# Kernel optimization log

Measured on AMD Instinct MI355X. Metric: run time of the kernel, lower is better.

Reference implementation:

```python
import jax, jax.numpy as jnp
import numpy as np

B, NIN, NREG, D, H, L = 8, 1024, 16, 1024, 16, 12
DFF = 4 * D
S = NIN + NREG
HD = D // H
EPS = 1e-6


def setup_inputs() -> dict:
    key = jax.random.key(0)
    ks = jax.random.split(key, 8)
    p = lambda k, shape: jax.random.normal(k, shape, jnp.float32) * 0.02
    return dict(
        x=jax.random.normal(ks[0], (B, S, D), jnp.float32),
        n_input=NIN,
        ln1_g=jnp.ones((L, D), jnp.float32), ln1_b=jnp.zeros((L, D), jnp.float32),
        wqkv=p(ks[1], (L, D, 3 * D)), bqkv=jnp.zeros((L, 3 * D), jnp.float32),
        wo=p(ks[2], (L, D, D)), bo=jnp.zeros((L, D), jnp.float32),
        ln2_g=jnp.ones((L, D), jnp.float32), ln2_b=jnp.zeros((L, D), jnp.float32),
        w1=p(ks[3], (L, D, DFF)), b1=jnp.zeros((L, DFF), jnp.float32),
        w2=p(ks[4], (L, DFF, D)), b2=jnp.zeros((L, D), jnp.float32),
        lnf_g=jnp.ones((D,), jnp.float32), lnf_b=jnp.zeros((D,), jnp.float32),
    )


def _ln(x, g, b):
    mu = x.mean(-1, keepdims=True)
    var = ((x - mu) ** 2).mean(-1, keepdims=True)
    return (x - mu) * jax.lax.rsqrt(var + EPS) * g + b


def _build_mask(n_input, total):
    # inputs attend everywhere; registers attend to all inputs and causally among registers
    i = jnp.arange(total)[:, None]
    j = jnp.arange(total)[None, :]
    blocked = (i >= n_input) & (j >= n_input) & (j > i)
    return jnp.where(blocked, -jnp.inf, 0.0).astype(jnp.float32)  # (S, S) additive


def _attn(h, wqkv_l, bqkv_l, wo_l, bo_l, mask):
    b, s, _ = h.shape
    qkv = h @ wqkv_l + bqkv_l                                   # (B,S,3D)
    q, k, v = jnp.split(qkv, 3, axis=-1)
    q = q.reshape(b, s, H, HD).transpose(0, 2, 1, 3)            # (B,H,S,HD)
    k = k.reshape(b, s, H, HD).transpose(0, 2, 1, 3)
    v = v.reshape(b, s, H, HD).transpose(0, 2, 1, 3)
    scores = jnp.einsum('bhqd,bhkd->bhqk', q, k) / np.sqrt(HD) + mask
    a = jax.nn.softmax(scores, axis=-1)
    o = jnp.einsum('bhqk,bhkd->bhqd', a, v)
    o = o.transpose(0, 2, 1, 3).reshape(b, s, D)
    return o @ wo_l + bo_l


def reference(x, n_input, ln1_g, ln1_b, wqkv, bqkv, wo, bo,
              ln2_g, ln2_b, w1, b1, w2, b2, lnf_g, lnf_b):
    mask = _build_mask(n_input, x.shape[1])

    def blk(h, p):
        l1g, l1b, wq, bq, wo_, bo_, l2g, l2b, w1_, b1_, w2_, b2_ = p
        h = h + _attn(_ln(h, l1g, l1b), wq, bq, wo_, bo_, mask)
        u = _ln(h, l2g, l2b) @ w1_ + b1_
        h = h + jax.nn.gelu(u) @ w2_ + b2_
        return h, None

    h, _ = jax.lax.scan(blk, x, (ln1_g, ln1_b, wqkv, bqkv, wo, bo,
                                 ln2_g, ln2_b, w1, b1, w2, b2))
    return _ln(h, lnf_g, lnf_b)
```

## Files before the change

### kernel.cpp

```cpp
#include <hip/hip_runtime.h>
#include <hip/hip_bf16.h>
#include <stdint.h>

#define DD   1024
#define TD   3072
#define DFFN 4096
#define NL   12
#define SS   1040
#define SP   1056
#define BB   8
#define MM   (BB*SS)
#define HH   16
#define NTAIL 16

typedef float  f32x4  __attribute__((ext_vector_type(4)));
typedef __bf16 bf16x8 __attribute__((ext_vector_type(8)));
typedef unsigned short u16;

union Bf8 { bf16x8 v; u16 s[8]; };

__device__ __forceinline__ u16 f2b(float f) {
  union { float f; unsigned u; } x; x.f = f;
  unsigned r = (x.u + 0x7FFFu + ((x.u >> 16) & 1u)) >> 16;
  return (u16)r;
}

__device__ __forceinline__ f32x4 mfma_bf16(bf16x8 a, bf16x8 b, f32x4 c) {
  return __builtin_amdgcn_mfma_f32_16x16x32_bf16(a, b, c, 0, 0, 0);
}

__device__ __forceinline__ void gload_lds16(const u16* g, u16* l) {
  __builtin_amdgcn_global_load_lds((const __attribute__((address_space(1))) void*)g,
                                   (__attribute__((address_space(3))) void*)l, 16, 0, 0);
}

__device__ __forceinline__ float dppmax16(float t) {
  union { float f; int i; } u, v;
  u.f = t;
  v.i = __builtin_amdgcn_update_dpp(0, u.i, 0xB1, 0xF, 0xF, true);
  u.f = fmaxf(u.f, v.f);
  v.i = __builtin_amdgcn_update_dpp(0, u.i, 0x4E, 0xF, 0xF, true);
  u.f = fmaxf(u.f, v.f);
  v.i = __builtin_amdgcn_update_dpp(0, u.i, 0x124, 0xF, 0xF, true);
  u.f = fmaxf(u.f, v.f);
  v.i = __builtin_amdgcn_update_dpp(0, u.i, 0x128, 0xF, 0xF, true);
  u.f = fmaxf(u.f, v.f);
  return u.f;
}

__global__ __launch_bounds__(256)
void transpose_cast(const float* __restrict__ in, u16* __restrict__ out, int K, int N) {
  __shared__ float tile[32][33];
  const int n0 = blockIdx.x * 32, k0 = blockIdx.y * 32;
  const size_t lb = (size_t)blockIdx.z * K * N;
  const int tx = threadIdx.x, ty = threadIdx.y;
  for (int j = 0; j < 4; ++j)
    tile[ty + 8*j][tx] = in[lb + (size_t)(k0 + ty + 8*j) * N + n0 + tx];
  __syncthreads();
  for (int j = 0; j < 4; ++j)
    out[lb + (size_t)(n0 + ty + 8*j) * K + k0 + tx] = f2b(tile[tx][ty + 8*j]);
}

template<int OUTF>
__global__ __launch_bounds__(256)
void ln_kernel(const float* __restrict__ in, const float* __restrict__ gam,
               const float* __restrict__ bet, u16* __restrict__ outb, float* __restrict__ outf) {
  const int row = blockIdx.x, t = threadIdx.x;
  const float4 v = ((const float4*)(in + (size_t)row * DD))[t];
  float s  = v.x + v.y + v.z + v.w;
  float s2 = v.x*v.x + v.y*v.y + v.z*v.z + v.w*v.w;
  for (int off = 1; off < 64; off <<= 1) { s += __shfl_xor(s, off); s2 += __shfl_xor(s2, off); }
  __shared__ float red[8];
  if ((t & 63) == 0) { red[t >> 6] = s; red[4 + (t >> 6)] = s2; }
  __syncthreads();
  s  = red[0] + red[1] + red[2] + red[3];
  s2 = red[4] + red[5] + red[6] + red[7];
  const float mu = s * (1.0f/1024.0f);
  const float var = s2 * (1.0f/1024.0f) - mu*mu;
  const float rs = rsqrtf(var + 1e-6f);
  const float4 gv = ((const float4*)gam)[t];
  const float4 bv = ((const float4*)bet)[t];
  const float y0 = (v.x - mu)*rs*gv.x + bv.x;
  const float y1 = (v.y - mu)*rs*gv.y + bv.y;
  const float y2 = (v.z - mu)*rs*gv.z + bv.z;
  const float y3 = (v.w - mu)*rs*gv.w + bv.w;
  if (OUTF) {
    float4 o; o.x=y0; o.y=y1; o.z=y2; o.w=y3;
    ((float4*)(outf + (size_t)row * DD))[t] = o;
  } else {
    ushort4 o; o.x=f2b(y0); o.y=f2b(y1); o.z=f2b(y2); o.w=f2b(y3);
    ((ushort4*)(outb + (size_t)row * DD))[t] = o;
  }
}

template<int EPI>
__global__ __launch_bounds__(256, 2)
void gemm_bt(const u16* __restrict__ A, const u16* __restrict__ Bt,
             const float* __restrict__ bias,
             u16* outB,
             u16* __restrict__ qb, u16* __restrict__ kb, u16* __restrict__ vtb,
             int N, int K) {
  __shared__ u16 As[128*64];
  __shared__ u16 Bs[128*64];
  const int tid = threadIdx.x;

  const int nwg = gridDim.x * gridDim.y;
  int wgid = blockIdx.y * gridDim.x + blockIdx.x;
  wgid = (wgid & 7) * (nwg >> 3) + (wgid >> 3);
  const int nb = wgid % gridDim.y;
  const int mb = wgid / gridDim.y;
  const int m0 = mb * 128, n0 = nb * 128;

  const int lane = tid & 63, w = tid >> 6;
  const int wr = (w >> 1) * 64, wc = (w & 1) * 64;
  const int c = lane & 15, g = lane >> 4;

  f32x4 acc[4][4];
  for (int i = 0; i < 4; ++i) for (int j = 0; j < 4; ++j) acc[i][j] = f32x4{0.f,0.f,0.f,0.f};

  const int srow = tid >> 3, scg = tid & 7;
  const size_t aoff = (size_t)(m0 + srow) * K + scg * 8;
  const size_t boff = (size_t)(n0 + srow) * K + scg * 8;

  for (int kt = 0; kt < K; kt += 64) {
    for (int it = 0; it < 4; ++it) {
      gload_lds16(A  + aoff + (size_t)it * 32 * K + kt, As + (it*256 + tid) * 8);
      gload_lds16(Bt + boff + (size_t)it * 32 * K + kt, Bs + (it*256 + tid) * 8);
    }
    __syncthreads();
    for (int kk = 0; kk < 2; ++kk) {
      bf16x8 af[4], bfr[4];
      for (int i = 0; i < 4; ++i) af[i]  = *(const bf16x8*)(As + (wr + i*16 + c)*64 + kk*32 + g*8);
      for (int j = 0; j < 4; ++j) bfr[j] = *(const bf16x8*)(Bs + (wc + j*16 + c)*64 + kk*32 + g*8);
      for (int i = 0; i < 4; ++i)
        for (int j = 0; j < 4; ++j)
          acc[i][j] = mfma_bf16(af[i], bfr[j], acc[i][j]);
    }
    __syncthreads();
  }

  for (int j = 0; j < 4; ++j) {
    const int col = n0 + wc + j*16 + c;
    const float bcol = bias[col];
    for (int i = 0; i < 4; ++i) {
      const int row0 = m0 + wr + i*16 + 4*g;
      if (EPI == 3) {
        const int part = col >> 10;
        const int hh2  = (col >> 6) & 15;
        const int hd   = col & 63;
        const int bb   = (int)((unsigned)row0 / SS);
        const int s0   = row0 - bb * SS;
        const size_t bh = (size_t)(bb * HH + hh2);
        if (part == 2) {
          ushort4 pk;
          pk.x = f2b(acc[i][j][0] + bcol);
          pk.y = f2b(acc[i][j][1] + bcol);
          pk.z = f2b(acc[i][j][2] + bcol);
          pk.w = f2b(acc[i][j][3] + bcol);
          *(ushort4*)(vtb + (bh*64 + hd)*SP + s0) = pk;
        } else if (part == 0) {
          for (int r = 0; r < 4; ++r)
            qb[(bh*SP + s0 + r)*64 + hd] = f2b((acc[i][j][r] + bcol) * 0.125f);
        } else {
          for (int r = 0; r < 4; ++r)
            kb[(bh*SP + s0 + r)*64 + hd] = f2b(acc[i][j][r] + bcol);
        }
      } else {
        for (int r = 0; r < 4; ++r) {
          const size_t idx = (size_t)(row0 + r) * N + col;
          const float v = acc[i][j][r] + bcol;
          const float z = 1.5957691216f * (v + 0.044715f * v * v * v);
          const float e = __expf(z);
          outB[idx] = f2b(v * e * __builtin_amdgcn_rcpf(e + 1.0f));
        }
      }
    }
  }
}

__global__ __launch_bounds__(256, 4)
void gemm64(const u16* __restrict__ A, const u16* __restrict__ Bt,
            const float* __restrict__ bias, const float* __restrict__ resid,
            float* __restrict__ outF, int N, int K) {
  __shared__ u16 As[64*64];
  __shared__ u16 Bs[128*64];
  const int tid = threadIdx.x;

  const int nwg = gridDim.x * gridDim.y;
  int wgid = blockIdx.y * gridDim.x + blockIdx.x;
  wgid = (wgid & 7) * (nwg >> 3) + (wgid >> 3);
  const int nb = wgid % gridDim.y;
  const int mb = wgid / gridDim.y;
  const int m0 = mb * 64, n0 = nb * 128;

  const int lane = tid & 63, w = tid >> 6;
  const int wr = (w >> 1) * 32, wc = (w & 1) * 64;
  const int c = lane & 15, g = lane >> 4;

  f32x4 acc[2][4];
  for (int i = 0; i < 2; ++i) for (int j = 0; j < 4; ++j) acc[i][j] = f32x4{0.f,0.f,0.f,0.f};

  const int srow = tid >> 3, scg = tid & 7;
  const size_t aoff = (size_t)(m0 + srow) * K + scg * 8;
  const size_t boff = (size_t)(n0 + srow) * K + scg * 8;

  for (int kt = 0; kt < K; kt += 64) {
    for (int it = 0; it < 2; ++it)
      gload_lds16(A  + aoff + (size_t)it * 32 * K + kt, As + (it*256 + tid) * 8);
    for (int it = 0; it < 4; ++it)
      gload_lds16(Bt + boff + (size_t)it * 32 * K + kt, Bs + (it*256 + tid) * 8);
    __syncthreads();
    for (int kk = 0; kk < 2; ++kk) {
      bf16x8 af[2], bfr[4];
      for (int i = 0; i < 2; ++i) af[i]  = *(const bf16x8*)(As + (wr + i*16 + c)*64 + kk*32 + g*8);
      for (int j = 0; j < 4; ++j) bfr[j] = *(const bf16x8*)(Bs + (wc + j*16 + c)*64 + kk*32 + g*8);
      for (int i = 0; i < 2; ++i)
        for (int j = 0; j < 4; ++j)
          acc[i][j] = mfma_bf16(af[i], bfr[j], acc[i][j]);
    }
    __syncthreads();
  }

  for (int j = 0; j < 4; ++j) {
    const int col = n0 + wc + j*16 + c;
    const float bcol = bias[col];
    for (int i = 0; i < 2; ++i) {
      const int row0 = m0 + wr + i*16 + 4*g;
      for (int r = 0; r < 4; ++r) {
        const size_t idx = (size_t)(row0 + r) * N + col;
        outF[idx] = acc[i][j][r] + bcol + resid[idx];
      }
    }
  }
}

__global__ __launch_bounds__(512, 8)
void attn_staged(const u16* __restrict__ Qb, const u16* __restrict__ Kb,
                 const u16* __restrict__ VTb, u16* __restrict__ out,
                 const int* __restrict__ npt) {
  __shared__ u16 KV[2][4096];
  __shared__ u16 PT[8][640];
  const int tid = threadIdx.x;
  const int w = tid >> 6, lane = tid & 63;
  const int c = lane & 15, g = lane >> 4;
  const int nin = npt[0];
  u16* pw = PT[w];

  if (blockIdx.x < NTAIL) {
    const int bh = blockIdx.x * 8 + w;
    const int b = bh >> 4, hh = bh & 15;
    const int q0 = 64 * 16;

    bf16x8 aq0, aq1;
    {
      const u16* qp = Qb + ((size_t)bh * SP + q0 + c) * 64 + g * 8;
      aq0 = *(const bf16x8*)qp;
      aq1 = *(const bf16x8*)(qp + 32);
    }

    float m[4], ls[4];
    f32x4 o[4];
    int qrow[4];
    for (int r = 0; r < 4; ++r) { m[r] = -1e30f; ls[r] = 0.f; qrow[r] = q0 + 4*g + r; }
    for (int nd = 0; nd < 4; ++nd) o[nd] = f32x4{0.f,0.f,0.f,0.f};

    for (int kt = 0; kt < 33; ++kt) {
      const int k0 = kt * 32;

      f32x4 s[2];
      {
        const u16* kp0 = Kb + ((size_t)bh * SP + k0 + c) * 64 + g * 8;
        f32x4 z0 = f32x4{0.f,0.f,0.f,0.f};
        z0 = mfma_bf16(aq0, *(const bf16x8*)kp0, z0);
        z0 = mfma_bf16(aq1, *(const bf16x8*)(kp0 + 32), z0);
        s[0] = z0;
        const u16* kp1 = kp0 + 16 * 64;
        f32x4 z1 = f32x4{0.f,0.f,0.f,0.f};
        z1 = mfma_bf16(aq0, *(const bf16x8*)kp1, z1);
        z1 = mfma_bf16(aq1, *(const bf16x8*)(kp1 + 32), z1);
        s[1] = z1;
      }

      for (int jt = 0; jt < 2; ++jt) {
        const int j = k0 + jt*16 + c;
        for (int r = 0; r < 4; ++r) {
          const int q = qrow[r];
          const bool blocked = (j >= SS) || ((q >= nin) && (j >= nin) && (j > q));
          if (blocked) s[jt][r] = -1e30f;
        }
      }

      for (int r = 0; r < 4; ++r) {
        float t = fmaxf(s[0][r], s[1][r]);
        for (int off = 1; off < 16; off <<= 1) t = fmaxf(t, __shfl_xor(t, off));
        const float mn = fmaxf(m[r], t);
        const float al = __expf(m[r] - mn);
        m[r] = mn;
        const float p0 = __expf(s[0][r] - mn);
        const float p1 = __expf(s[1][r] - mn);
        s[0][r] = p0; s[1][r] = p1;
        float ps = p0 + p1;
        for (int off = 1; off < 16; off <<= 1) ps += __shfl_xor(ps, off);
        ls[r] = ls[r] * al + ps;
        for (int nd = 0; nd < 4; ++nd) o[nd][r] *= al;
      }

      for (int jt = 0; jt < 2; ++jt)
        for (int r = 0; r < 4; ++r)
          pw[(4*g + r)*40 + jt*16 + c] = f2b(s[jt][r]);
      __builtin_amdgcn_sched_barrier(0);
      bf16x8 ap = *(const bf16x8*)(pw + c*40 + 8*g);
      __builtin_amdgcn_sched_barrier(0);

      for (int nd = 0; nd < 4; ++nd) {
        const u16* vp = VTb + ((size_t)bh * 64 + nd*16 + c) * SP + k0 + 8*g;
        o[nd] = mfma_bf16(ap, *(const bf16x8*)vp, o[nd]);
      }
    }

    for (int nd = 0; nd < 4; ++nd)
      for (int r = 0; r < 4; ++r) {
        const float v = o[nd][r] / ls[r];
        out[((size_t)b * SS + qrow[r]) * DD + hh*64 + nd*16 + c] = f2b(v);
      }
    return;
  }

  const int sb = blockIdx.x - NTAIL;
  const int bh = sb & 127;
  const int qt = (sb >> 7) * 8 + w;
  const int b = bh >> 4, hh = bh & 15;
  const int q0 = qt * 16;

  const u16* ssrc; int kstr; u16* sdst;
  if (tid < 256) {
    const int row = tid >> 3, col8 = (tid & 7) ^ (row & 7);
    ssrc = Kb + ((size_t)bh * SP + row) * 64 + col8 * 8;
    kstr = 32 * 64;
    sdst = &KV[0][tid * 8];
  } else {
    const int t2 = tid - 256, row = t2 >> 2, col8 = (t2 & 3) ^ (row & 3);
    ssrc = VTb + ((size_t)bh * 64 + row) * SP + col8 * 8;
    kstr = 32;
    sdst = &KV[0][2048 + t2 * 8];
  }
#define STAGE(bufbit, kt) gload_lds16(ssrc + (size_t)(kt) * kstr, sdst + (bufbit) * 4096)

  bf16x8 aq0, aq1;
  {
    const u16* qp = Qb + ((size_t)bh * SP + q0 + c) * 64 + g * 8;
    aq0 = *(const bf16x8*)qp;
    aq1 = *(const bf16x8*)(qp + 32);
  }

  Bf8 onesf;
  for (int i = 0; i < 8; ++i) onesf.s[i] = (c == 0) ? (u16)0x3F80 : (u16)0;

  float m[4];
  f32x4 o[5];
  int qrow[4];
  for (int r = 0; r < 4; ++r) { m[r] = -1e30f; qrow[r] = q0 + 4*g + r; }
  for (int nd = 0; nd < 5; ++nd) o[nd] = f32x4{0.f,0.f,0.f,0.f};

  const bool tile_regs = (q0 + 15) >= nin;
  const int c7 = c & 7, c3 = c & 3;

  STAGE(0, 0);

  for (int kt = 0; kt < 33; ++kt) {
    const int buf = kt & 1;
    __syncthreads();
    if (kt < 32) STAGE(buf ^ 1, kt + 1);
    const u16* Kt = &KV[buf][0];
    const u16* Vt = &KV[buf][2048];
    const int k0 = kt * 32;

    f32x4 s[2];
    {
      bf16x8 k00 = *(const bf16x8*)(Kt + c*64        + ((g    ) ^ c7) * 8);
      bf16x8 k01 = *(const bf16x8*)(Kt + c*64        + ((g + 4) ^ c7) * 8);
      f32x4 z0 = f32x4{0.f,0.f,0.f,0.f};
      z0 = mfma_bf16(aq0, k00, z0);
      z0 = mfma_bf16(aq1, k01, z0);
      s[0] = z0;
      bf16x8 k10 = *(const bf16x8*)(Kt + (c+16)*64   + ((g    ) ^ c7) * 8);
      bf16x8 k11 = *(const bf16x8*)(Kt + (c+16)*64   + ((g + 4) ^ c7) * 8);
      f32x4 z1 = f32x4{0.f,0.f,0.f,0.f};
      z1 = mfma_bf16(aq0, k10, z1);
      z1 = mfma_bf16(aq1, k11, z1);
      s[1] = z1;
    }

    if (tile_regs || (k0 + 31 >= SS)) {
      for (int jt = 0; jt < 2; ++jt) {
        const int j = k0 + jt*16 + c;
        for (int r = 0; r < 4; ++r) {
          const int q = qrow[r];
          const bool blocked = (j >= SS) || ((q >= nin) && (j >= nin) && (j > q));
          if (blocked) s[jt][r] = -1e30f;
        }
      }
    }

    for (int r = 0; r < 4; ++r) {
      const float t = dppmax16(fmaxf(s[0][r], s[1][r]));
      const float mn = fmaxf(m[r], t);
      const float al = __expf(m[r] - mn);
      m[r] = mn;
      for (int nd = 0; nd < 5; ++nd) o[nd][r] *= al;
      s[0][r] = __expf(s[0][r] - mn);
      s[1][r] = __expf(s[1][r] - mn);
    }

    for (int jt = 0; jt < 2; ++jt)
      for (int r = 0; r < 4; ++r)
        pw[(4*g + r)*40 + jt*16 + c] = f2b(s[jt][r]);
    __builtin_amdgcn_sched_barrier(0);
    bf16x8 ap = *(const bf16x8*)(pw + c*40 + 8*g);
    __builtin_amdgcn_sched_barrier(0);

    for (int nd = 0; nd < 4; ++nd) {
      bf16x8 bv = *(const bf16x8*)(Vt + (nd*16 + c)*32 + ((g ^ c3) * 8));
      o[nd] = mfma_bf16(ap, bv, o[nd]);
    }
    o[4] = mfma_bf16(ap, onesf.v, o[4]);
  }
#undef STAGE

  float rls[4];
  for (int r = 0; r < 4; ++r)
    rls[r] = 1.0f / __shfl(o[4][r], lane & 48);
  for (int nd = 0; nd < 4; ++nd)
    for (int r = 0; r < 4; ++r)
      out[((size_t)b * SS + qrow[r]) * DD + hh*64 + nd*16 + c] = f2b(o[nd][r] * rls[r]);
}

extern "C" void kernel_launch(void* const* d_in, const int* in_sizes, int n_in,
                              void* d_out, int out_size, void* d_ws, size_t ws_size,
                              hipStream_t stream) {
  const float* x    = (const float*)d_in[0];
  const int*   npt  = (const int*)  d_in[1];
  const float* ln1g = (const float*)d_in[2];
  const float* ln1b = (const float*)d_in[3];
  const float* wqkv = (const float*)d_in[4];
  const float* bqkv = (const float*)d_in[5];
  const float* wo   = (const float*)d_in[6];
  const float* bo   = (const float*)d_in[7];
  const float* ln2g = (const float*)d_in[8];
  const float* ln2b = (const float*)d_in[9];
  const float* w1   = (const float*)d_in[10];
  const float* b1   = (const float*)d_in[11];
  const float* w2   = (const float*)d_in[12];
  const float* b2   = (const float*)d_in[13];
  const float* lnfg = (const float*)d_in[14];
  const float* lnfb = (const float*)d_in[15];

  char* ws = (char*)d_ws;
  size_t off = 0;
  u16*   wqkvT = (u16*)(ws + off);   off += (size_t)NL*TD*DD*2;
  u16*   woT   = (u16*)(ws + off);   off += (size_t)NL*DD*DD*2;
  u16*   w1T   = (u16*)(ws + off);   off += (size_t)NL*DFFN*DD*2;
  u16*   w2T   = (u16*)(ws + off);   off += (size_t)NL*DD*DFFN*2;
  float* h     = (float*)(ws + off); off += (size_t)MM*DD*4;
  u16*   lnb   = (u16*)(ws + off);   off += (size_t)MM*DD*2;
  u16*   Qb    = (u16*)(ws + off);   off += (size_t)BB*HH*SP*64*2;
  u16*   Kb    = (u16*)(ws + off);   off += (size_t)BB*HH*SP*64*2;
  u16*   VTb   = (u16*)(ws + off);   off += (size_t)BB*HH*64*SP*2;
  u16*   attnO = (u16*)(ws + off);   off += (size_t)MM*DD*2;
  u16*   ffh   = (u16*)(ws + off);   off += (size_t)MM*DFFN*2;

  const dim3 tb(32, 8);
  transpose_cast<<<dim3(TD/32,   DD/32,   NL), tb, 0, stream>>>(wqkv, wqkvT, DD,   TD);
  transpose_cast<<<dim3(DD/32,   DD/32,   NL), tb, 0, stream>>>(wo,   woT,   DD,   DD);
  transpose_cast<<<dim3(DFFN/32, DD/32,   NL), tb, 0, stream>>>(w1,   w1T,   DD,   DFFN);
  transpose_cast<<<dim3(DD/32,   DFFN/32, NL), tb, 0, stream>>>(w2,   w2T,   DFFN, DD);
  hipMemcpyAsync(h, x, (size_t)MM*DD*4, hipMemcpyDeviceToDevice, stream);
  hipMemsetAsync(Qb, 0, (size_t)3*BB*HH*SP*64*2, stream);

  for (int l = 0; l < NL; ++l) {
    ln_kernel<0><<<MM, 256, 0, stream>>>(h, ln1g + (size_t)l*DD, ln1b + (size_t)l*DD, lnb, nullptr);
    gemm_bt<3><<<dim3(MM/128, TD/128), 256, 0, stream>>>(
        lnb, wqkvT + (size_t)l*TD*DD, bqkv + (size_t)l*TD, nullptr,
        Qb, Kb, VTb, TD, DD);
    attn_staged<<<dim3(BB*HH*8 + NTAIL), 512, 0, stream>>>(Qb, Kb, VTb, attnO, npt);
    gemm64<<<dim3(MM/64, DD/128), 256, 0, stream>>>(
        attnO, woT + (size_t)l*DD*DD, bo + (size_t)l*DD, h, h, DD, DD);
    ln_kernel<0><<<MM, 256, 0, stream>>>(h, ln2g + (size_t)l*DD, ln2b + (size_t)l*DD, lnb, nullptr);
    gemm_bt<1><<<dim3(MM/128, DFFN/128), 256, 0, stream>>>(
        lnb, w1T + (size_t)l*DFFN*DD, b1 + (size_t)l*DFFN, ffh,
        nullptr, nullptr, nullptr, DFFN, DD);
    gemm64<<<dim3(MM/64, DD/128), 256, 0, stream>>>(
        ffh, w2T + (size_t)l*DD*DFFN, b2 + (size_t)l*DD, h, h, DD, DFFN);
  }
  ln_kernel<1><<<MM, 256, 0, stream>>>(h, lnfg, lnfb, nullptr, (float*)d_out);
}
```

Baseline: 6.156 ms.

## Process two query tiles per attention wave and use 128x128 GEMM for FFN down-projection

The attention kernel now has each wave handle two 16-row query tiles against every staged K/V tile. This halves the number of blocks (512 instead of 1024) and reuses each LDS K fragment load for two sets of MFMAs, at the cost of more registers; launch bounds drop occupancy from 8 to 4 waves. Separately, the FFN second GEMM (K=4096) moves from the 64-row gemm64 kernel to the 128x128 gemm_bt tile with a new fp32 residual-add epilogue, raising arithmetic intensity but launching fewer workgroups (520 instead of 1040).

```diff
diff --git a/kernel.cpp b/kernel.cpp
--- a/kernel.cpp
+++ b/kernel.cpp
@@ -96,8 +96,8 @@
 template<int EPI>
 __global__ __launch_bounds__(256, 2)
 void gemm_bt(const u16* __restrict__ A, const u16* __restrict__ Bt,
-             const float* __restrict__ bias,
-             u16* outB,
+             const float* __restrict__ bias, const float* __restrict__ resid,
+             float* outF, u16* outB,
              u16* __restrict__ qb, u16* __restrict__ kb, u16* __restrict__ vtb,
              int N, int K) {
   __shared__ u16 As[128*64];
@@ -169,9 +169,13 @@
         for (int r = 0; r < 4; ++r) {
           const size_t idx = (size_t)(row0 + r) * N + col;
           const float v = acc[i][j][r] + bcol;
-          const float z = 1.5957691216f * (v + 0.044715f * v * v * v);
-          const float e = __expf(z);
-          outB[idx] = f2b(v * e * __builtin_amdgcn_rcpf(e + 1.0f));
+          if (EPI == 1) {
+            const float z = 1.5957691216f * (v + 0.044715f * v * v * v);
+            const float e = __expf(z);
+            outB[idx] = f2b(v * e * __builtin_amdgcn_rcpf(e + 1.0f));
+          } else {
+            outF[idx] = v + resid[idx];
+          }
         }
       }
     }
@@ -234,7 +238,7 @@
   }
 }
 
-__global__ __launch_bounds__(512, 8)
+__global__ __launch_bounds__(512, 4)
 void attn_staged(const u16* __restrict__ Qb, const u16* __restrict__ Kb,
                  const u16* __restrict__ VTb, u16* __restrict__ out,
                  const int* __restrict__ npt) {
@@ -328,9 +332,8 @@
 
   const int sb = blockIdx.x - NTAIL;
   const int bh = sb & 127;
-  const int qt = (sb >> 7) * 8 + w;
+  const int qg = sb >> 7;
   const int b = bh >> 4, hh = bh & 15;
-  const int q0 = qt * 16;
 
   const u16* ssrc; int kstr; u16* sdst;
   if (tid < 256) {
@@ -346,23 +349,28 @@
   }
 #define STAGE(bufbit, kt) gload_lds16(ssrc + (size_t)(kt) * kstr, sdst + (bufbit) * 4096)
 
-  bf16x8 aq0, aq1;
-  {
-    const u16* qp = Qb + ((size_t)bh * SP + q0 + c) * 64 + g * 8;
-    aq0 = *(const bf16x8*)qp;
-    aq1 = *(const bf16x8*)(qp + 32);
+  bf16x8 aq[2][2];
+  int q0[2];
+#pragma unroll
+  for (int qq = 0; qq < 2; ++qq) {
+    q0[qq] = (qg * 16 + w * 2 + qq) * 16;
+    const u16* qp = Qb + ((size_t)bh * SP + q0[qq] + c) * 64 + g * 8;
+    aq[qq][0] = *(const bf16x8*)qp;
+    aq[qq][1] = *(const bf16x8*)(qp + 32);
   }
 
   Bf8 onesf;
   for (int i = 0; i < 8; ++i) onesf.s[i] = (c == 0) ? (u16)0x3F80 : (u16)0;
 
-  float m[4];
-  f32x4 o[5];
-  int qrow[4];
-  for (int r = 0; r < 4; ++r) { m[r] = -1e30f; qrow[r] = q0 + 4*g + r; }
-  for (int nd = 0; nd < 5; ++nd) o[nd] = f32x4{0.f,0.f,0.f,0.f};
-
-  const bool tile_regs = (q0 + 15) >= nin;
+  float m[2][4];
+  f32x4 o[2][5];
+#pragma unroll
+  for (int qq = 0; qq < 2; ++qq) {
+    for (int r = 0; r < 4; ++r) m[qq][r] = -1e30f;
+    for (int nd = 0; nd < 5; ++nd) o[qq][nd] = f32x4{0.f,0.f,0.f,0.f};
+  }
+  const bool tregs0 = (q0[0] + 15) >= nin;
+  const bool tregs1 = (q0[1] + 15) >= nin;
   const int c7 = c & 7, c3 = c & 3;
 
   STAGE(0, 0);
@@ -375,64 +383,74 @@
     const u16* Vt = &KV[buf][2048];
     const int k0 = kt * 32;
 
-    f32x4 s[2];
-    {
-      bf16x8 k00 = *(const bf16x8*)(Kt + c*64        + ((g    ) ^ c7) * 8);
-      bf16x8 k01 = *(const bf16x8*)(Kt + c*64        + ((g + 4) ^ c7) * 8);
-      f32x4 z0 = f32x4{0.f,0.f,0.f,0.f};
-      z0 = mfma_bf16(aq0, k00, z0);
-      z0 = mfma_bf16(aq1, k01, z0);
-      s[0] = z0;
-      bf16x8 k10 = *(const bf16x8*)(Kt + (c+16)*64   + ((g    ) ^ c7) * 8);
-      bf16x8 k11 = *(const bf16x8*)(Kt + (c+16)*64   + ((g + 4) ^ c7) * 8);
-      f32x4 z1 = f32x4{0.f,0.f,0.f,0.f};
-      z1 = mfma_bf16(aq0, k10, z1);
-      z1 = mfma_bf16(aq1, k11, z1);
-      s[1] = z1;
-    }
-
-    if (tile_regs || (k0 + 31 >= SS)) {
-      for (int jt = 0; jt < 2; ++jt) {
-        const int j = k0 + jt*16 + c;
-        for (int r = 0; r < 4; ++r) {
-          const int q = qrow[r];
-          const bool blocked = (j >= SS) || ((q >= nin) && (j >= nin) && (j > q));
-          if (blocked) s[jt][r] = -1e30f;
+    bf16x8 k00 = *(const bf16x8*)(Kt + c*64        + ((g    ) ^ c7) * 8);
+    bf16x8 k01 = *(const bf16x8*)(Kt + c*64        + ((g + 4) ^ c7) * 8);
+    bf16x8 k10 = *(const bf16x8*)(Kt + (c+16)*64   + ((g    ) ^ c7) * 8);
+    bf16x8 k11 = *(const bf16x8*)(Kt + (c+16)*64   + ((g + 4) ^ c7) * 8);
+
+#pragma unroll
+    for (int qq = 0; qq < 2; ++qq) {
+      f32x4 s[2];
+      {
+        f32x4 z0 = f32x4{0.f,0.f,0.f,0.f};
+        z0 = mfma_bf16(aq[qq][0], k00, z0);
+        z0 = mfma_bf16(aq[qq][1], k01, z0);
+        s[0] = z0;
+        f32x4 z1 = f32x4{0.f,0.f,0.f,0.f};
+        z1 = mfma_bf16(aq[qq][0], k10, z1);
+        z1 = mfma_bf16(aq[qq][1], k11, z1);
+        s[1] = z1;
+      }
+
+      const bool tregs = qq ? tregs1 : tregs0;
+      if (tregs || (k0 + 31 >= SS)) {
+        const int qr0 = q0[qq] + 4*g;
+        for (int jt = 0; jt < 2; ++jt) {
+          const int j = k0 + jt*16 + c;
+          for (int r = 0; r < 4; ++r) {
+            const int q = qr0 + r;
+            const bool blocked = (j >= SS) || ((q >= nin) && (j >= nin) && (j > q));
+            if (blocked) s[jt][r] = -1e30f;
+          }
         }
       }
-    }
-
-    for (int r = 0; r < 4; ++r) {
-      const float t = dppmax16(fmaxf(s[0][r], s[1][r]));
-      const float mn = fmaxf(m[r], t);
-      const float al = __expf(m[r] - mn);
-      m[r] = mn;
-      for (int nd = 0; nd < 5; ++nd) o[nd][r] *= al;
-      s[0][r] = __expf(s[0][r] - mn);
-      s[1][r] = __expf(s[1][r] - mn);
-    }
-
-    for (int jt = 0; jt < 2; ++jt)
+
+      for (int r = 0; r < 4; ++r) {
+        const float t = dppmax16(fmaxf(s[0][r], s[1][r]));
+        const float mn = fmaxf(m[qq][r], t);
+        const float al = __expf(m[qq][r] - mn);
+        m[qq][r] = mn;
+        for (int nd = 0; nd < 5; ++nd) o[qq][nd][r] *= al;
+        s[0][r] = __expf(s[0][r] - mn);
+        s[1][r] = __expf(s[1][r] - mn);
+      }
+
+      for (int jt = 0; jt < 2; ++jt)
+        for (int r = 0; r < 4; ++r)
+          pw[(4*g + r)*40 + jt*16 + c] = f2b(s[jt][r]);
+      __builtin_amdgcn_sched_barrier(0);
+      bf16x8 ap = *(const bf16x8*)(pw + c*40 + 8*g);
+      __builtin_amdgcn_sched_barrier(0);
+
+      for (int nd = 0; nd < 4; ++nd) {
+        bf16x8 bv = *(const bf16x8*)(Vt + (nd*16 + c)*32 + ((g ^ c3) * 8));
+        o[qq][nd] = mfma_bf16(ap, bv, o[qq][nd]);
+      }
+      o[qq][4] = mfma_bf16(ap, onesf.v, o[qq][4]);
+    }
+  }
+#undef STAGE
+
+#pragma unroll
+  for (int qq = 0; qq < 2; ++qq) {
+    float rls[4];
+    for (int r = 0; r < 4; ++r)
+      rls[r] = 1.0f / __shfl(o[qq][4][r], lane & 48);
+    const int qr0 = q0[qq] + 4*g;
+    for (int nd = 0; nd < 4; ++nd)
       for (int r = 0; r < 4; ++r)
-        pw[(4*g + r)*40 + jt*16 + c] = f2b(s[jt][r]);
-    __builtin_amdgcn_sched_barrier(0);
-    bf16x8 ap = *(const bf16x8*)(pw + c*40 + 8*g);
-    __builtin_amdgcn_sched_barrier(0);
-
-    for (int nd = 0; nd < 4; ++nd) {
-      bf16x8 bv = *(const bf16x8*)(Vt + (nd*16 + c)*32 + ((g ^ c3) * 8));
-      o[nd] = mfma_bf16(ap, bv, o[nd]);
-    }
-    o[4] = mfma_bf16(ap, onesf.v, o[4]);
-  }
-#undef STAGE
-
-  float rls[4];
-  for (int r = 0; r < 4; ++r)
-    rls[r] = 1.0f / __shfl(o[4][r], lane & 48);
-  for (int nd = 0; nd < 4; ++nd)
-    for (int r = 0; r < 4; ++r)
-      out[((size_t)b * SS + qrow[r]) * DD + hh*64 + nd*16 + c] = f2b(o[nd][r] * rls[r]);
+        out[((size_t)b * SS + qr0 + r) * DD + hh*64 + nd*16 + c] = f2b(o[qq][nd][r] * rls[r]);
+  }
 }
 
 extern "C" void kernel_launch(void* const* d_in, const int* in_sizes, int n_in,
@@ -480,17 +498,18 @@
   for (int l = 0; l < NL; ++l) {
     ln_kernel<0><<<MM, 256, 0, stream>>>(h, ln1g + (size_t)l*DD, ln1b + (size_t)l*DD, lnb, nullptr);
     gemm_bt<3><<<dim3(MM/128, TD/128), 256, 0, stream>>>(
-        lnb, wqkvT + (size_t)l*TD*DD, bqkv + (size_t)l*TD, nullptr,
+        lnb, wqkvT + (size_t)l*TD*DD, bqkv + (size_t)l*TD, nullptr, nullptr, nullptr,
         Qb, Kb, VTb, TD, DD);
-    attn_staged<<<dim3(BB*HH*8 + NTAIL), 512, 0, stream>>>(Qb, Kb, VTb, attnO, npt);
+    attn_staged<<<dim3(512 + NTAIL), 512, 0, stream>>>(Qb, Kb, VTb, attnO, npt);
     gemm64<<<dim3(MM/64, DD/128), 256, 0, stream>>>(
         attnO, woT + (size_t)l*DD*DD, bo + (size_t)l*DD, h, h, DD, DD);
     ln_kernel<0><<<MM, 256, 0, stream>>>(h, ln2g + (size_t)l*DD, ln2b + (size_t)l*DD, lnb, nullptr);
     gemm_bt<1><<<dim3(MM/128, DFFN/128), 256, 0, stream>>>(
-        lnb, w1T + (size_t)l*DFFN*DD, b1 + (size_t)l*DFFN, ffh,
+        lnb, w1T + (size_t)l*DFFN*DD, b1 + (size_t)l*DFFN, nullptr, nullptr, ffh,
         nullptr, nullptr, nullptr, DFFN, DD);
-    gemm64<<<dim3(MM/64, DD/128), 256, 0, stream>>>(
-        ffh, w2T + (size_t)l*DD*DFFN, b2 + (size_t)l*DD, h, h, DD, DFFN);
+    gemm_bt<2><<<dim3(MM/128, DD/128), 256, 0, stream>>>(
+        ffh, w2T + (size_t)l*DD*DFFN, b2 + (size_t)l*DD, h, h, nullptr,
+        nullptr, nullptr, nullptr, DD, DFFN);
   }
   ln_kernel<1><<<MM, 256, 0, stream>>>(h, lnfg, lnfb, nullptr, (float*)d_out);
 }
```

New measurement: 6.112 ms. No clear change (-0.7%).
